# Kernel tuning notes

Measured on AMD Instinct MI355X. Metric: run time of the kernel, lower is better.

Reference implementation:

```python
import jax, jax.numpy as jnp
import numpy as np

N = 50000
E = 800000
F_IN = 128
HID = 64
HEADS = 4
P = 16384


def setup_inputs() -> dict:
    key = jax.random.key(0)
    ks = jax.random.split(key, 20)
    s = 0.05
    inp = {
        'x': jax.random.normal(ks[0], (N, F_IN), jnp.float32),
        'edge_src': jax.random.randint(ks[1], (E,), 0, N, jnp.int32),
        'edge_dst': jax.random.randint(ks[2], (E,), 0, N, jnp.int32),
        'edge_attr': jax.random.uniform(ks[3], (E, 1), jnp.float32),
        'pair_indices': jax.random.randint(ks[4], (P, 2), 0, N, jnp.int32),
        # conv1: in=F_IN, heads=4, out=HID, edge_dim=1
        'W1': jax.random.normal(ks[5], (F_IN, HEADS * HID), jnp.float32) * s,
        'We1': jax.random.normal(ks[6], (1, HEADS * HID), jnp.float32) * s,
        'as1': jax.random.normal(ks[7], (HEADS, HID), jnp.float32) * s,
        'ad1': jax.random.normal(ks[8], (HEADS, HID), jnp.float32) * s,
        'ae1': jax.random.normal(ks[9], (HEADS, HID), jnp.float32) * s,
        'b1': jnp.zeros((HEADS * HID,), jnp.float32),
        # conv2: in=4*HID, heads=1, out=HID
        'W2': jax.random.normal(ks[10], (HEADS * HID, HID), jnp.float32) * s,
        'We2': jax.random.normal(ks[11], (1, HID), jnp.float32) * s,
        'as2': jax.random.normal(ks[12], (1, HID), jnp.float32) * s,
        'ad2': jax.random.normal(ks[13], (1, HID), jnp.float32) * s,
        'ae2': jax.random.normal(ks[14], (1, HID), jnp.float32) * s,
        'b2': jnp.zeros((HID,), jnp.float32),
        'Wlin': jax.random.normal(ks[15], (2 * HID, 1), jnp.float32) * s,
        'blin': jnp.zeros((1,), jnp.float32),
    }
    return inp


def gat_conv(x, src, dst, edge_attr, W, We, att_src, att_dst, att_edge, bias, heads, C):
    """PyG GATConv (add_self_loops=True, fill_value='mean', negative_slope=0.2, eval mode)."""
    n = x.shape[0]
    # self-loop edge_attr = mean of incoming edge attrs per node
    deg = jax.ops.segment_sum(jnp.ones_like(dst, dtype=edge_attr.dtype), dst, num_segments=n)
    loop_attr = jax.ops.segment_sum(edge_attr, dst, num_segments=n) / jnp.maximum(deg, 1.0)[:, None]
    loop = jnp.arange(n, dtype=src.dtype)
    src_f = jnp.concatenate([src, loop])
    dst_f = jnp.concatenate([dst, loop])
    ea = jnp.concatenate([edge_attr, loop_attr], axis=0)  # [E+N, 1]
    h = (x @ W).reshape(n, heads, C)                      # [N, H, C]
    a_src = (h * att_src).sum(-1)                         # [N, H]
    a_dst = (h * att_dst).sum(-1)
    e = (ea @ We).reshape(-1, heads, C)                   # [E+N, H, C]
    a_edge = (e * att_edge).sum(-1)                       # [E+N, H]
    alpha = jax.nn.leaky_relu(a_src[src_f] + a_dst[dst_f] + a_edge, 0.2)
    amax = jax.ops.segment_max(alpha, dst_f, num_segments=n)
    ex = jnp.exp(alpha - amax[dst_f])
    denom = jax.ops.segment_sum(ex, dst_f, num_segments=n)
    w = ex / denom[dst_f]                                 # segment softmax over dst
    msg = h[src_f] * w[..., None]                         # [E+N, H, C]
    out = jax.ops.segment_sum(msg, dst_f, num_segments=n) # [N, H, C]
    return out.reshape(n, heads * C) + bias


def reference(x, edge_src, edge_dst, edge_attr, pair_indices,
              W1, We1, as1, ad1, ae1, b1,
              W2, We2, as2, ad2, ae2, b2, Wlin, blin):
    # dropout is identity in eval mode
    h1 = jax.nn.elu(gat_conv(x, edge_src, edge_dst, edge_attr,
                             W1, We1, as1, ad1, ae1, b1, HEADS, HID))
    h2 = gat_conv(h1, edge_src, edge_dst, edge_attr,
                  W2, We2, as2, ad2, ae2, b2, 1, HID)
    d1 = h2[pair_indices[:, 0]]
    d2 = h2[pair_indices[:, 1]]
    pf = jnp.concatenate([d1, d2], axis=1)                # [P, 2*HID]
    return jax.nn.sigmoid(pf @ Wlin + blin).reshape(-1)
```

## Files before the change

### kernel.cpp

```cpp
#include <hip/hip_runtime.h>
#include <hip/hip_fp16.h>
#include <math.h>

typedef __attribute__((ext_vector_type(8))) short short8;
typedef __attribute__((ext_vector_type(4))) float floatx4;
typedef __attribute__((ext_vector_type(2))) float float2v;

__device__ __forceinline__ unsigned short f2bf(float f){
  unsigned int x = __float_as_uint(f);
  unsigned int r = x + 0x7fff + ((x >> 16) & 1);
  return (unsigned short)(r >> 16);
}
__device__ __forceinline__ unsigned char f2fp8(float v){
  int pk = __builtin_amdgcn_cvt_pk_fp8_f32(v, 0.f, 0, false);
  return (unsigned char)(pk & 0xff);
}
__device__ __forceinline__ float wsumf(float v){
#pragma unroll
  for (int o = 32; o; o >>= 1) v += __shfl_xor(v, o, 64);
  return v;
}

__global__ __launch_bounds__(256) void k_count(const int* __restrict__ dst,
    const float* __restrict__ eattr, unsigned long long* __restrict__ degp,
    int* __restrict__ rank, int E, int N){
  int e = blockIdx.x * 256 + threadIdx.x;
  if (e >= E) return;
  int b = blockIdx.x & 7;
  int d = dst[e];
  unsigned long long add = (1ull << 40) |
      (unsigned long long)(eattr[e] * 16777216.0f);
  unsigned long long old = atomicAdd(&degp[(size_t)b * N + d], add);
  rank[e] = (int)(old >> 40);
}

__global__ __launch_bounds__(256) void k_scan1(const unsigned long long* __restrict__ degp,
    int* __restrict__ row_ptr, int* __restrict__ bsum, int n){
  __shared__ int sm[2][256];
  int tid = threadIdx.x, gid = blockIdx.x * 256 + tid;
  int v = 0;
  if (gid < n){
#pragma unroll
    for (int b = 0; b < 8; b++) v += (int)(degp[(size_t)b * n + gid] >> 40);
  }
  sm[0][tid] = v; __syncthreads();
  int pin = 0;
  for (int off = 1; off < 256; off <<= 1){
    int t = sm[pin][tid];
    if (tid >= off) t += sm[pin][tid - off];
    sm[pin ^ 1][tid] = t; pin ^= 1; __syncthreads();
  }
  int incl = sm[pin][tid];
  if (gid < n) row_ptr[gid] = incl - v;
  if (tid == 255) bsum[blockIdx.x] = incl;
}

__global__ __launch_bounds__(256) void k_scan2(const int* __restrict__ bsum,
    int* __restrict__ bofs, int nb){
  __shared__ int sm[2][256];
  int tid = threadIdx.x;
  int v = (tid < nb) ? bsum[tid] : 0;
  sm[0][tid] = v; __syncthreads();
  int pin = 0;
  for (int off = 1; off < 256; off <<= 1){
    int t = sm[pin][tid];
    if (tid >= off) t += sm[pin][tid - off];
    sm[pin ^ 1][tid] = t; pin ^= 1; __syncthreads();
  }
  bofs[tid] = sm[pin][tid] - v;
}

__global__ __launch_bounds__(256) void k_scan3(int* __restrict__ row_ptr,
    const int* __restrict__ bofs, const unsigned long long* __restrict__ degp,
    float* __restrict__ lattr, int* __restrict__ base, int n, int E){
  int gid = blockIdx.x * 256 + threadIdx.x;
  if (gid >= n) return;
  int rp = row_ptr[gid] + bofs[gid >> 8];
  row_ptr[gid] = rp;
  const unsigned long long M40 = (1ull << 40) - 1;
  int cum = 0; float s = 0.f;
  int bb[8];
#pragma unroll
  for (int b = 0; b < 8; b++){
    unsigned long long p = degp[(size_t)b * n + gid];
    bb[b] = rp + cum;
    cum += (int)(p >> 40);
    s += (float)(p & M40);
  }
  lattr[gid] = (s * (1.0f / 16777216.0f)) / fmaxf((float)cum, 1.0f);
  int4* bp = (int4*)(base + (size_t)gid * 8);
  bp[0] = make_int4(bb[0], bb[1], bb[2], bb[3]);
  bp[1] = make_int4(bb[4], bb[5], bb[6], bb[7]);
  if (gid == 0) row_ptr[n] = E;
}

__global__ __launch_bounds__(256) void k_scatter(const int* __restrict__ src,
    const int* __restrict__ dst, const float* __restrict__ eattr,
    const int* __restrict__ rank, const int* __restrict__ base,
    int2* __restrict__ csr, int E){
  int e = blockIdx.x * 256 + threadIdx.x;
  if (e >= E) return;
  int b = blockIdx.x & 7;
  int d = dst[e];
  int pos = base[(size_t)d * 8 + b] + rank[e];
  csr[pos] = make_int2(src[e], __float_as_int(eattr[e]));
}

__global__ void k_prep(const float* __restrict__ W1, const float* __restrict__ as1,
    const float* __restrict__ ad1, const float* __restrict__ W2,
    const float* __restrict__ as2, const float* __restrict__ ad2,
    const float* __restrict__ We1, const float* __restrict__ ae1,
    const float* __restrict__ We2, const float* __restrict__ ae2,
    const float* __restrict__ b2, const float* __restrict__ Wlin,
    unsigned short* __restrict__ W1p, float* __restrict__ w2vT,
    float* __restrict__ ce){
  int b = blockIdx.x, lane = threadIdx.x;
  if (b < 68){
    int nt = b >> 2, kc = b & 3;
    int col = lane & 15, krow = kc * 32 + (lane >> 4) * 8;
    unsigned short tmp[8];
    if (nt < 16){
#pragma unroll
      for (int j = 0; j < 8; j++) tmp[j] = f2bf(W1[(size_t)(krow + j) * 256 + nt * 16 + col]);
    } else {
#pragma unroll
      for (int j = 0; j < 8; j++){
        float v = 0.f;
        if (col < 8){
          const float* av = (col < 4) ? as1 : ad1;
          int h = col & 3;
          for (int c = 0; c < 64; c++)
            v += W1[(size_t)(krow + j) * 256 + h * 64 + c] * av[h * 64 + c];
        }
        tmp[j] = f2bf(v);
      }
    }
    unsigned short* dstp = W1p + (((size_t)nt * 4 + kc) * 64 + lane) * 8;
    *(ushort4*)(dstp)     = make_ushort4(tmp[0], tmp[1], tmp[2], tmp[3]);
    *(ushort4*)(dstp + 4) = make_ushort4(tmp[4], tmp[5], tmp[6], tmp[7]);
  } else if (b < 72){
    int k = (b - 68) * 64 + lane;
    float4 a = make_float4(0.f, 0.f, 0.f, 0.f);
    for (int c = 0; c < 64; c++){
      float wv = W2[(size_t)k * 64 + c];
      a.x += wv * as2[c];
      a.y += wv * ad2[c];
      a.z += wv * Wlin[c];
      a.w += wv * Wlin[64 + c];
    }
    w2vT[k]       = a.x;
    w2vT[256 + k] = a.y;
    w2vT[512 + k] = a.z;
    w2vT[768 + k] = a.w;
  } else {
    float p0 = We1[lane]       * ae1[lane];
    float p1 = We1[64 + lane]  * ae1[64 + lane];
    float p2 = We1[128 + lane] * ae1[128 + lane];
    float p3 = We1[192 + lane] * ae1[192 + lane];
    float p4 = We2[lane]       * ae2[lane];
    float c1 = b2[lane] * Wlin[lane];
    float c2 = b2[lane] * Wlin[64 + lane];
    p0 = wsumf(p0); p1 = wsumf(p1); p2 = wsumf(p2); p3 = wsumf(p3); p4 = wsumf(p4);
    c1 = wsumf(c1); c2 = wsumf(c2);
    if (lane == 0){
      ce[0] = p0; ce[1] = p1; ce[2] = p2; ce[3] = p3; ce[4] = p4;
      ce[5] = c1; ce[6] = c2;
    }
  }
}

__global__ __launch_bounds__(256) void k_gemm1_att(const float* __restrict__ A,
    const unsigned short* __restrict__ Bp, unsigned char* __restrict__ h1f8,
    float* __restrict__ asrc, float* __restrict__ adst, int M){
  constexpr int K = 128, NKC = 4;
  __shared__ unsigned short Bs[256 * K];
  {
    const uint4* srcp = (const uint4*)Bp;
    uint4* dstp = (uint4*)Bs;
    for (int i = threadIdx.x; i < 4096; i += 256) dstp[i] = srcp[i];
  }
  __syncthreads();
  int wave = threadIdx.x >> 6, lane = threadIdx.x & 63;
  int quad = lane >> 4, col = lane & 15;
  int r0 = (blockIdx.x * 4 + wave) * 16;
  int rowc = min(r0 + col, M - 1);
  short8 af[NKC], sf[NKC];
#pragma unroll
  for (int kc = 0; kc < NKC; kc++){
    float4 a0 = *(const float4*)(A + (size_t)rowc * K + kc * 32 + quad * 8);
    float4 a1 = *(const float4*)(A + (size_t)rowc * K + kc * 32 + quad * 8 + 4);
    short8 t;
    t[0] = (short)f2bf(a0.x); t[1] = (short)f2bf(a0.y);
    t[2] = (short)f2bf(a0.z); t[3] = (short)f2bf(a0.w);
    t[4] = (short)f2bf(a1.x); t[5] = (short)f2bf(a1.y);
    t[6] = (short)f2bf(a1.z); t[7] = (short)f2bf(a1.w);
    af[kc] = t;
    sf[kc] = *(const short8*)(Bp + (((size_t)16 * 4 + kc) * 64 + lane) * 8);
  }
  floatx4 acc[17];
#pragma unroll
  for (int nt = 0; nt < 17; nt++) acc[nt] = (floatx4){0.f, 0.f, 0.f, 0.f};
#pragma unroll
  for (int kc = 0; kc < NKC; kc++){
#pragma unroll
    for (int nt = 0; nt < 16; nt++){
      short8 bfv = *(const short8*)(&Bs[((nt * NKC + kc) * 64 + lane) * 8]);
      acc[nt] = __builtin_amdgcn_mfma_f32_16x16x32_bf16(af[kc], bfv, acc[nt], 0, 0, 0);
    }
    acc[16] = __builtin_amdgcn_mfma_f32_16x16x32_bf16(af[kc], sf[kc], acc[16], 0, 0, 0);
  }
#pragma unroll
  for (int nt = 0; nt < 16; nt++){
#pragma unroll
    for (int i = 0; i < 4; i++){
      int r = r0 + quad * 4 + i;
      if (r < M) h1f8[(size_t)r * 256 + nt * 16 + col] = f2fp8(acc[nt][i]);
    }
  }
#pragma unroll
  for (int i = 0; i < 4; i++){
    int r = r0 + quad * 4 + i;
    if (r < M){
      float v = acc[16][i];
      if (col < 4)      asrc[(size_t)r * 4 + col] = v;
      else if (col < 8) adst[(size_t)r * 4 + (col - 4)] = v;
    }
  }
}

__global__ __launch_bounds__(256) void k_gat1(
    const int* __restrict__ row_ptr, const int2* __restrict__ csr,
    const float* __restrict__ lattr,
    const float* __restrict__ a_src, const float* __restrict__ a_dst,
    const float* __restrict__ ce, const unsigned char* __restrict__ hpre,
    const float* __restrict__ bias, const float* __restrict__ w2vT,
    float4* __restrict__ upd, int n){
  int node = blockIdx.x * 4 + (threadIdx.x >> 6);
  if (node >= n) return;
  int lane = threadIdx.x & 63;
  int q = lane >> 4, lsub = lane & 15, hq = lsub >> 2;
  int start = row_ptr[node], deg = row_ptr[node + 1] - start;
  float4 as4 = *(const float4*)(a_src + (size_t)node * 4);
  float4 ad4 = *(const float4*)(a_dst + (size_t)node * 4);
  float4 ce4 = *(const float4*)ce;
  float la = lattr[node];
  float4 wv4[4];
#pragma unroll
  for (int j = 0; j < 4; j++)
    wv4[j] = *(const float4*)(w2vT + (size_t)lane * 16 + j * 4);
  float asvh = hq == 0 ? as4.x : hq == 1 ? as4.y : hq == 2 ? as4.z : as4.w;
  float advh = hq == 0 ? ad4.x : hq == 1 ? ad4.y : hq == 2 ? ad4.z : ad4.w;
  float ceh  = hq == 0 ? ce4.x : hq == 1 ? ce4.y : hq == 2 ? ce4.z : ce4.w;
  float2v acc2[8];
#pragma unroll
  for (int k = 0; k < 8; k++) acc2[k] = (float2v){0.f, 0.f};
  float dn = 0.f;
  if (q == 0){
    float aself = asvh + advh + la * ceh;
    aself = aself > 0.f ? aself : 0.2f * aself;
    float wself = __expf(aself);
    dn = wself;
    uint4 u = *(const uint4*)(hpre + (size_t)node * 256 + lsub * 16);
    float2v w2 = (float2v){wself, wself};
    unsigned uu[4] = {u.x, u.y, u.z, u.w};
#pragma unroll
    for (int j = 0; j < 4; j++){
      acc2[2 * j]     = w2 * __builtin_amdgcn_cvt_pk_f32_fp8((int)uu[j], false);
      acc2[2 * j + 1] = w2 * __builtin_amdgcn_cvt_pk_f32_fp8((int)uu[j], true);
    }
  }
  for (int e = q; e < deg; e += 8){
    bool vB = (e + 4) < deg;
    int2 seA = csr[start + e];
    int2 seB = csr[start + (vB ? e + 4 : e)];
    float aA = a_src[(size_t)seA.x * 4 + hq] + advh + __int_as_float(seA.y) * ceh;
    aA = aA > 0.f ? aA : 0.2f * aA;
    float wA = __expf(aA);
    float aB = a_src[(size_t)seB.x * 4 + hq] + advh + __int_as_float(seB.y) * ceh;
    aB = aB > 0.f ? aB : 0.2f * aB;
    float wB = vB ? __expf(aB) : 0.f;
    uint4 uA = *(const uint4*)(hpre + (size_t)seA.x * 256 + lsub * 16);
    uint4 uB = *(const uint4*)(hpre + (size_t)seB.x * 256 + lsub * 16);
    dn += wA + wB;
    float2v wA2 = (float2v){wA, wA}, wB2 = (float2v){wB, wB};
    unsigned ua[4] = {uA.x, uA.y, uA.z, uA.w};
    unsigned ub[4] = {uB.x, uB.y, uB.z, uB.w};
#pragma unroll
    for (int j = 0; j < 4; j++){
      acc2[2 * j]     += wA2 * __builtin_amdgcn_cvt_pk_f32_fp8((int)ua[j], false);
      acc2[2 * j + 1] += wA2 * __builtin_amdgcn_cvt_pk_f32_fp8((int)ua[j], true);
      acc2[2 * j]     += wB2 * __builtin_amdgcn_cvt_pk_f32_fp8((int)ub[j], false);
      acc2[2 * j + 1] += wB2 * __builtin_amdgcn_cvt_pk_f32_fp8((int)ub[j], true);
    }
  }
  dn += __shfl_xor(dn, 16, 64);
  dn += __shfl_xor(dn, 32, 64);
#pragma unroll
  for (int k = 0; k < 8; k++){
    acc2[k].x += __shfl_xor(acc2[k].x, 16, 64);
    acc2[k].x += __shfl_xor(acc2[k].x, 32, 64);
    acc2[k].y += __shfl_xor(acc2[k].y, 16, 64);
    acc2[k].y += __shfl_xor(acc2[k].y, 32, 64);
  }
  {
    float inv = 1.f / dn;
    float d = 0.f;
#pragma unroll
    for (int j = 0; j < 4; j++){
      float4 b4 = *(const float4*)(bias + lsub * 16 + j * 4);
      float bbv[4] = {b4.x, b4.y, b4.z, b4.w};
      float wvv[4] = {wv4[j].x, wv4[j].y, wv4[j].z, wv4[j].w};
#pragma unroll
      for (int t = 0; t < 4; t++){
        int k = j * 4 + t;
        float av = (k & 1) ? acc2[k >> 1].y : acc2[k >> 1].x;
        float v = av * inv + bbv[t];
        v = v > 0.f ? v : (__expf(v) - 1.f);
        d += v * wvv[t];
      }
    }
#pragma unroll
    for (int o = 1; o < 16; o <<= 1) d += __shfl_xor(d, o, 64);
    if (lsub == 0) ((float*)&upd[node])[q] = d;
  }
}

__global__ __launch_bounds__(256) void k_gat2(
    const int* __restrict__ row_ptr, const int2* __restrict__ csr,
    const float* __restrict__ lattr, const float4* __restrict__ upd,
    const float* __restrict__ ce,
    float* __restrict__ s1v, float* __restrict__ s2v, int n){
  int node = blockIdx.x * 32 + (threadIdx.x >> 3);
  if (node >= n) return;
  int lane8 = threadIdx.x & 7;
  int start = row_ptr[node], deg = row_ptr[node + 1] - start;
  float4 own = upd[node];
  float ad = own.y, c = ce[4];
  float t1 = 0.f, t2 = 0.f, dn = 0.f;
  if (lane8 == 0){
    float a = own.x + ad + lattr[node] * c;
    a = a > 0.f ? a : 0.2f * a;
    float w = __expf(a);
    dn = w; t1 = w * own.z; t2 = w * own.w;
  }
  for (int e = lane8; e < deg; e += 8){
    int2 se = csr[start + e];
    float4 o = upd[se.x];
    float a = o.x + ad + __int_as_float(se.y) * c;
    a = a > 0.f ? a : 0.2f * a;
    float w = __expf(a);
    dn += w; t1 += w * o.z; t2 += w * o.w;
  }
#pragma unroll
  for (int o = 1; o < 8; o <<= 1){
    dn += __shfl_xor(dn, o, 64);
    t1 += __shfl_xor(t1, o, 64);
    t2 += __shfl_xor(t2, o, 64);
  }
  if (lane8 == 0){
    float inv = 1.f / dn;
    s1v[node] = t1 * inv + ce[5];
    s2v[node] = t2 * inv + ce[6];
  }
}

__global__ __launch_bounds__(256) void k_pairs(const int* __restrict__ pairs,
    const float* __restrict__ s1v, const float* __restrict__ s2v,
    const float* __restrict__ blin, float* __restrict__ out, int P){
  int p = blockIdx.x * 256 + threadIdx.x;
  if (p >= P) return;
  int i = pairs[2 * p], j = pairs[2 * p + 1];
  float x = s1v[i] + s2v[j] + blin[0];
  out[p] = 1.f / (1.f + __expf(-x));
}

extern "C" void kernel_launch(void* const* d_in, const int* in_sizes, int n_in,
                              void* d_out, int out_size, void* d_ws, size_t ws_size,
                              hipStream_t stream) {
  const float* x     = (const float*)d_in[0];
  const int*   esrc  = (const int*)  d_in[1];
  const int*   edst  = (const int*)  d_in[2];
  const float* eattr = (const float*)d_in[3];
  const int*   pairs = (const int*)  d_in[4];
  const float* W1    = (const float*)d_in[5];
  const float* We1   = (const float*)d_in[6];
  const float* as1   = (const float*)d_in[7];
  const float* ad1   = (const float*)d_in[8];
  const float* ae1   = (const float*)d_in[9];
  const float* b1    = (const float*)d_in[10];
  const float* W2    = (const float*)d_in[11];
  const float* We2   = (const float*)d_in[12];
  const float* as2   = (const float*)d_in[13];
  const float* ad2   = (const float*)d_in[14];
  const float* ae2   = (const float*)d_in[15];
  const float* b2    = (const float*)d_in[16];
  const float* Wlin  = (const float*)d_in[17];
  const float* blin  = (const float*)d_in[18];
  float* out = (float*)d_out;

  const int N = in_sizes[0] / 128;
  const int E = in_sizes[1];
  const int P = in_sizes[4] / 2;

  char* w = (char*)d_ws;
  size_t off = 0;
  auto alloc = [&](size_t bytes) -> size_t {
    size_t r = off; off = (off + bytes + 255) & ~(size_t)255; return r;
  };
  size_t o_degp   = alloc((size_t)N * 64);
  size_t zero_end = off;
  size_t o_rank   = alloc((size_t)E * 4);
  size_t o_rowptr = alloc((size_t)(N + 1) * 4);
  size_t o_bsum   = alloc(1024);
  size_t o_bofs   = alloc(1024);
  size_t o_lattr  = alloc((size_t)N * 4);
  size_t o_base   = alloc((size_t)N * 32);
  size_t o_csr    = alloc((size_t)E * 8);
  size_t o_asrc1  = alloc((size_t)N * 16);
  size_t o_adst1  = alloc((size_t)N * 16);
  size_t o_upd    = alloc((size_t)N * 16);
  size_t o_ce     = alloc(64);
  size_t o_s1     = alloc((size_t)N * 4);
  size_t o_s2     = alloc((size_t)N * 4);
  size_t o_W1p    = alloc((size_t)17 * 4 * 64 * 8 * 2);
  size_t o_w2v    = alloc(256 * 16);
  size_t o_h1f8   = alloc((size_t)N * 256);
  (void)ws_size;

  unsigned long long* degp = (unsigned long long*)(w + o_degp);
  int*   rank   = (int*)  (w + o_rank);
  int*   rowptr = (int*)  (w + o_rowptr);
  int*   bsum   = (int*)  (w + o_bsum);
  int*   bofs   = (int*)  (w + o_bofs);
  float* lattr  = (float*)(w + o_lattr);
  int*   base   = (int*)  (w + o_base);
  int2*  csr    = (int2*) (w + o_csr);
  float* asrc1  = (float*)(w + o_asrc1);
  float* adst1  = (float*)(w + o_adst1);
  float4* upd   = (float4*)(w + o_upd);
  float* ce     = (float*)(w + o_ce);
  float* s1v    = (float*)(w + o_s1);
  float* s2v    = (float*)(w + o_s2);
  unsigned short* W1p = (unsigned short*)(w + o_W1p);
  float* w2vT   = (float*)(w + o_w2v);
  unsigned char* h1f8 = (unsigned char*)(w + o_h1f8);

  hipMemsetAsync(w, 0, zero_end, stream);

  int ebl = (E + 255) / 256;
  int nbl = (N + 255) / 256;
  int wbl = (N + 3) / 4;

  k_count<<<ebl, 256, 0, stream>>>(edst, eattr, degp, rank, E, N);
  k_scan1<<<nbl, 256, 0, stream>>>(degp, rowptr, bsum, N);
  k_scan2<<<1, 256, 0, stream>>>(bsum, bofs, nbl);
  k_scan3<<<nbl, 256, 0, stream>>>(rowptr, bofs, degp, lattr, base, N, E);
  k_scatter<<<ebl, 256, 0, stream>>>(esrc, edst, eattr, rank, base, csr, E);

  k_prep<<<73, 64, 0, stream>>>(W1, as1, ad1, W2, as2, ad2,
                                We1, ae1, We2, ae2, b2, Wlin, W1p, w2vT, ce);

  k_gemm1_att<<<(N + 63) / 64, 256, 0, stream>>>(x, W1p, h1f8, asrc1, adst1, N);
  k_gat1<<<wbl, 256, 0, stream>>>(rowptr, csr, lattr, asrc1, adst1, ce,
                                  h1f8, b1, w2vT, upd, N);
  k_gat2<<<(N + 31) / 32, 256, 0, stream>>>(rowptr, csr, lattr, upd, ce,
                                            s1v, s2v, N);
  k_pairs<<<(P + 255) / 256, 256, 0, stream>>>(pairs, s1v, s2v, blin, out, P);
}
```

Baseline: 258.9 us.

## Pack CSR entries into 32 bits, shrink rank to bytes, fold scan2 into scan3

Each CSR entry now stores a 16-bit source index plus the edge attribute as fp16 in one 32-bit word instead of an int2, which halves CSR traffic in scatter, gat1 and gat2. The per-edge rank is stored as a byte rather than an int. The separate single-block scan2 launch is removed, and each scan3 block reduces the preceding block sums itself. The bias loads in gat1 are hoisted out of the epilogue loop. The packing assumes node ids below 65536 and per-bucket ranks below 256, and it rounds edge attributes to fp16, which holds for these sizes but is fragile and less precise.

```diff
diff --git a/kernel.cpp b/kernel.cpp
--- a/kernel.cpp
+++ b/kernel.cpp
@@ -23,7 +23,7 @@
 
 __global__ __launch_bounds__(256) void k_count(const int* __restrict__ dst,
     const float* __restrict__ eattr, unsigned long long* __restrict__ degp,
-    int* __restrict__ rank, int E, int N){
+    unsigned char* __restrict__ rank, int E, int N){
   int e = blockIdx.x * 256 + threadIdx.x;
   if (e >= E) return;
   int b = blockIdx.x & 7;
@@ -31,7 +31,7 @@
   unsigned long long add = (1ull << 40) |
       (unsigned long long)(eattr[e] * 16777216.0f);
   unsigned long long old = atomicAdd(&degp[(size_t)b * N + d], add);
-  rank[e] = (int)(old >> 40);
+  rank[e] = (unsigned char)(old >> 40);
 }
 
 __global__ __launch_bounds__(256) void k_scan1(const unsigned long long* __restrict__ degp,
@@ -55,27 +55,20 @@
   if (tid == 255) bsum[blockIdx.x] = incl;
 }
 
-__global__ __launch_bounds__(256) void k_scan2(const int* __restrict__ bsum,
-    int* __restrict__ bofs, int nb){
-  __shared__ int sm[2][256];
+__global__ __launch_bounds__(256) void k_scan3(int* __restrict__ row_ptr,
+    const int* __restrict__ bsum, const unsigned long long* __restrict__ degp,
+    float* __restrict__ lattr, int* __restrict__ base, int n, int E){
   int tid = threadIdx.x;
-  int v = (tid < nb) ? bsum[tid] : 0;
-  sm[0][tid] = v; __syncthreads();
-  int pin = 0;
-  for (int off = 1; off < 256; off <<= 1){
-    int t = sm[pin][tid];
-    if (tid >= off) t += sm[pin][tid - off];
-    sm[pin ^ 1][tid] = t; pin ^= 1; __syncthreads();
-  }
-  bofs[tid] = sm[pin][tid] - v;
-}
-
-__global__ __launch_bounds__(256) void k_scan3(int* __restrict__ row_ptr,
-    const int* __restrict__ bofs, const unsigned long long* __restrict__ degp,
-    float* __restrict__ lattr, int* __restrict__ base, int n, int E){
-  int gid = blockIdx.x * 256 + threadIdx.x;
+  int partial = (tid < (int)blockIdx.x) ? bsum[tid] : 0;
+#pragma unroll
+  for (int o = 32; o; o >>= 1) partial += __shfl_xor(partial, o, 64);
+  __shared__ int ws[4];
+  if ((tid & 63) == 0) ws[tid >> 6] = partial;
+  __syncthreads();
+  int blockOfs = ws[0] + ws[1] + ws[2] + ws[3];
+  int gid = blockIdx.x * 256 + tid;
   if (gid >= n) return;
-  int rp = row_ptr[gid] + bofs[gid >> 8];
+  int rp = row_ptr[gid] + blockOfs;
   row_ptr[gid] = rp;
   const unsigned long long M40 = (1ull << 40) - 1;
   int cum = 0; float s = 0.f;
@@ -96,14 +89,16 @@
 
 __global__ __launch_bounds__(256) void k_scatter(const int* __restrict__ src,
     const int* __restrict__ dst, const float* __restrict__ eattr,
-    const int* __restrict__ rank, const int* __restrict__ base,
-    int2* __restrict__ csr, int E){
+    const unsigned char* __restrict__ rank, const int* __restrict__ base,
+    unsigned* __restrict__ csrp, int E){
   int e = blockIdx.x * 256 + threadIdx.x;
   if (e >= E) return;
   int b = blockIdx.x & 7;
   int d = dst[e];
-  int pos = base[(size_t)d * 8 + b] + rank[e];
-  csr[pos] = make_int2(src[e], __float_as_int(eattr[e]));
+  int pos = base[(size_t)d * 8 + b] + (int)rank[e];
+  unsigned u = (unsigned)src[e] |
+      ((unsigned)__half_as_ushort(__float2half_rn(eattr[e])) << 16);
+  csrp[pos] = u;
 }
 
 __global__ void k_prep(const float* __restrict__ W1, const float* __restrict__ as1,
@@ -229,7 +224,7 @@
 }
 
 __global__ __launch_bounds__(256) void k_gat1(
-    const int* __restrict__ row_ptr, const int2* __restrict__ csr,
+    const int* __restrict__ row_ptr, const unsigned* __restrict__ csrp,
     const float* __restrict__ lattr,
     const float* __restrict__ a_src, const float* __restrict__ a_dst,
     const float* __restrict__ ce, const unsigned char* __restrict__ hpre,
@@ -244,10 +239,12 @@
   float4 ad4 = *(const float4*)(a_dst + (size_t)node * 4);
   float4 ce4 = *(const float4*)ce;
   float la = lattr[node];
-  float4 wv4[4];
-#pragma unroll
-  for (int j = 0; j < 4; j++)
+  float4 wv4[4], bb4[4];
+#pragma unroll
+  for (int j = 0; j < 4; j++){
     wv4[j] = *(const float4*)(w2vT + (size_t)lane * 16 + j * 4);
+    bb4[j] = *(const float4*)(bias + lsub * 16 + j * 4);
+  }
   float asvh = hq == 0 ? as4.x : hq == 1 ? as4.y : hq == 2 ? as4.z : as4.w;
   float advh = hq == 0 ? ad4.x : hq == 1 ? ad4.y : hq == 2 ? ad4.z : ad4.w;
   float ceh  = hq == 0 ? ce4.x : hq == 1 ? ce4.y : hq == 2 ? ce4.z : ce4.w;
@@ -271,16 +268,19 @@
   }
   for (int e = q; e < deg; e += 8){
     bool vB = (e + 4) < deg;
-    int2 seA = csr[start + e];
-    int2 seB = csr[start + (vB ? e + 4 : e)];
-    float aA = a_src[(size_t)seA.x * 4 + hq] + advh + __int_as_float(seA.y) * ceh;
+    unsigned uA_ = csrp[start + e];
+    unsigned uB_ = csrp[start + (vB ? e + 4 : e)];
+    int sA = (int)(uA_ & 0xffffu), sB = (int)(uB_ & 0xffffu);
+    float eaA = __half2float(__ushort_as_half((unsigned short)(uA_ >> 16)));
+    float eaB = __half2float(__ushort_as_half((unsigned short)(uB_ >> 16)));
+    float aA = a_src[(size_t)sA * 4 + hq] + advh + eaA * ceh;
     aA = aA > 0.f ? aA : 0.2f * aA;
     float wA = __expf(aA);
-    float aB = a_src[(size_t)seB.x * 4 + hq] + advh + __int_as_float(seB.y) * ceh;
+    float aB = a_src[(size_t)sB * 4 + hq] + advh + eaB * ceh;
     aB = aB > 0.f ? aB : 0.2f * aB;
     float wB = vB ? __expf(aB) : 0.f;
-    uint4 uA = *(const uint4*)(hpre + (size_t)seA.x * 256 + lsub * 16);
-    uint4 uB = *(const uint4*)(hpre + (size_t)seB.x * 256 + lsub * 16);
+    uint4 uA = *(const uint4*)(hpre + (size_t)sA * 256 + lsub * 16);
+    uint4 uB = *(const uint4*)(hpre + (size_t)sB * 256 + lsub * 16);
     dn += wA + wB;
     float2v wA2 = (float2v){wA, wA}, wB2 = (float2v){wB, wB};
     unsigned ua[4] = {uA.x, uA.y, uA.z, uA.w};
@@ -307,8 +307,7 @@
     float d = 0.f;
 #pragma unroll
     for (int j = 0; j < 4; j++){
-      float4 b4 = *(const float4*)(bias + lsub * 16 + j * 4);
-      float bbv[4] = {b4.x, b4.y, b4.z, b4.w};
+      float bbv[4] = {bb4[j].x, bb4[j].y, bb4[j].z, bb4[j].w};
       float wvv[4] = {wv4[j].x, wv4[j].y, wv4[j].z, wv4[j].w};
 #pragma unroll
       for (int t = 0; t < 4; t++){
@@ -326,7 +325,7 @@
 }
 
 __global__ __launch_bounds__(256) void k_gat2(
-    const int* __restrict__ row_ptr, const int2* __restrict__ csr,
+    const int* __restrict__ row_ptr, const unsigned* __restrict__ csrp,
     const float* __restrict__ lattr, const float4* __restrict__ upd,
     const float* __restrict__ ce,
     float* __restrict__ s1v, float* __restrict__ s2v, int n){
@@ -344,9 +343,11 @@
     dn = w; t1 = w * own.z; t2 = w * own.w;
   }
   for (int e = lane8; e < deg; e += 8){
-    int2 se = csr[start + e];
-    float4 o = upd[se.x];
-    float a = o.x + ad + __int_as_float(se.y) * c;
+    unsigned u = csrp[start + e];
+    int s = (int)(u & 0xffffu);
+    float ea = __half2float(__ushort_as_half((unsigned short)(u >> 16)));
+    float4 o = upd[s];
+    float a = o.x + ad + ea * c;
     a = a > 0.f ? a : 0.2f * a;
     float w = __expf(a);
     dn += w; t1 += w * o.z; t2 += w * o.w;
@@ -409,13 +410,12 @@
   };
   size_t o_degp   = alloc((size_t)N * 64);
   size_t zero_end = off;
-  size_t o_rank   = alloc((size_t)E * 4);
+  size_t o_rank   = alloc((size_t)E);
   size_t o_rowptr = alloc((size_t)(N + 1) * 4);
   size_t o_bsum   = alloc(1024);
-  size_t o_bofs   = alloc(1024);
   size_t o_lattr  = alloc((size_t)N * 4);
   size_t o_base   = alloc((size_t)N * 32);
-  size_t o_csr    = alloc((size_t)E * 8);
+  size_t o_csr    = alloc((size_t)E * 4);
   size_t o_asrc1  = alloc((size_t)N * 16);
   size_t o_adst1  = alloc((size_t)N * 16);
   size_t o_upd    = alloc((size_t)N * 16);
@@ -428,13 +428,12 @@
   (void)ws_size;
 
   unsigned long long* degp = (unsigned long long*)(w + o_degp);
-  int*   rank   = (int*)  (w + o_rank);
+  unsigned char* rank = (unsigned char*)(w + o_rank);
   int*   rowptr = (int*)  (w + o_rowptr);
   int*   bsum   = (int*)  (w + o_bsum);
-  int*   bofs   = (int*)  (w + o_bofs);
   float* lattr  = (float*)(w + o_lattr);
   int*   base   = (int*)  (w + o_base);
-  int2*  csr    = (int2*) (w + o_csr);
+  unsigned* csrp = (unsigned*)(w + o_csr);
   float* asrc1  = (float*)(w + o_asrc1);
   float* adst1  = (float*)(w + o_adst1);
   float4* upd   = (float4*)(w + o_upd);
@@ -453,17 +452,16 @@
 
   k_count<<<ebl, 256, 0, stream>>>(edst, eattr, degp, rank, E, N);
   k_scan1<<<nbl, 256, 0, stream>>>(degp, rowptr, bsum, N);
-  k_scan2<<<1, 256, 0, stream>>>(bsum, bofs, nbl);
-  k_scan3<<<nbl, 256, 0, stream>>>(rowptr, bofs, degp, lattr, base, N, E);
-  k_scatter<<<ebl, 256, 0, stream>>>(esrc, edst, eattr, rank, base, csr, E);
+  k_scan3<<<nbl, 256, 0, stream>>>(rowptr, bsum, degp, lattr, base, N, E);
+  k_scatter<<<ebl, 256, 0, stream>>>(esrc, edst, eattr, rank, base, csrp, E);
 
   k_prep<<<73, 64, 0, stream>>>(W1, as1, ad1, W2, as2, ad2,
                                 We1, ae1, We2, ae2, b2, Wlin, W1p, w2vT, ce);
 
   k_gemm1_att<<<(N + 63) / 64, 256, 0, stream>>>(x, W1p, h1f8, asrc1, adst1, N);
-  k_gat1<<<wbl, 256, 0, stream>>>(rowptr, csr, lattr, asrc1, adst1, ce,
+  k_gat1<<<wbl, 256, 0, stream>>>(rowptr, csrp, lattr, asrc1, adst1, ce,
                                   h1f8, b1, w2vT, upd, N);
-  k_gat2<<<(N + 31) / 32, 256, 0, stream>>>(rowptr, csr, lattr, upd, ce,
+  k_gat2<<<(N + 31) / 32, 256, 0, stream>>>(rowptr, csrp, lattr, upd, ce,
                                             s1v, s2v, N);
   k_pairs<<<(P + 255) / 256, 256, 0, stream>>>(pairs, s1v, s2v, blin, out, P);
 }
```

After: 277.5 us. +7.2%, slower.
